# Kernel optimization log

Hardware: AMD Instinct MI355X
Metric: run time of the kernel (lower is better)

The kernel has to match this reference:

```python
import jax, jax.numpy as jnp
import numpy as np

E = 1024   # embd_size
H = 16     # heads_num
DH = E // H
DFF = 4 * E
B, T = 2, 2048


def layer_norm(x, g, b, eps=1e-5):
    mu = jnp.mean(x, axis=-1, keepdims=True)
    var = jnp.var(x, axis=-1, keepdims=True)
    return (x - mu) * jax.lax.rsqrt(var + eps) * g + b


def setup_inputs() -> dict:
    key = jax.random.key(0)
    ks = jax.random.split(key, 12)
    s = 0.02
    return {
        "x": jax.random.normal(ks[0], (B, T, E), dtype=jnp.float32),
        "Wq": jax.random.normal(ks[1], (E, E), dtype=jnp.float32) * s,
        "Wk": jax.random.normal(ks[2], (E, E), dtype=jnp.float32) * s,
        "Wv": jax.random.normal(ks[3], (E, E), dtype=jnp.float32) * s,
        "Wo": jax.random.normal(ks[4], (E, E), dtype=jnp.float32) * s,
        "bo": jnp.zeros((E,), dtype=jnp.float32),
        "W1": jax.random.normal(ks[5], (E, DFF), dtype=jnp.float32) * s,
        "b1": jnp.zeros((DFF,), dtype=jnp.float32),
        "W2": jax.random.normal(ks[6], (DFF, E), dtype=jnp.float32) * s,
        "b2": jnp.zeros((E,), dtype=jnp.float32),
        "g1": jnp.ones((E,), dtype=jnp.float32),
        "be1": jnp.zeros((E,), dtype=jnp.float32),
        "g2": jnp.ones((E,), dtype=jnp.float32),
        "be2": jnp.zeros((E,), dtype=jnp.float32),
    }


def reference(x, Wq, Wk, Wv, Wo, bo, W1, b1, W2, b2, g1, be1, g2, be2):
    Bx, Tx, C = x.shape
    # --- self-attention sublayer ---
    h = layer_norm(x, g1, be1)
    # per-head projections; heads concatenated along output dim == stacked weights
    q = (h @ Wq).reshape(Bx, Tx, H, DH)  # [B,T,H,Dh]
    k = (h @ Wk).reshape(Bx, Tx, H, DH)
    v = (h @ Wv).reshape(Bx, Tx, H, DH)
    # NOTE: original scales by full embd_size**-0.5 (C = x.shape[-1]), not head_size
    scale = C ** (-0.5)
    scores = jnp.einsum("bqhd,bkhd->bhqk", q, k) * scale  # [B,H,T,T]
    mask = jnp.tril(jnp.ones((Tx, Tx), dtype=bool))
    scores = jnp.where(mask, scores, -jnp.inf)
    attn = jax.nn.softmax(scores, axis=-1)
    o = jnp.einsum("bhqk,bkhd->bqhd", attn, v).reshape(Bx, Tx, C)
    sa = o @ Wo + bo
    x = x + sa
    # --- feed-forward sublayer ---
    h2 = layer_norm(x, g2, be2)
    ff = jax.nn.relu(h2 @ W1 + b1) @ W2 + b2
    return x + ff
```

## Files before the change

### kernel.cpp

```cpp
#include <hip/hip_runtime.h>
#include <hip/hip_bf16.h>
#include <math.h>

#define Bn 2
#define Tn 2048
#define En 1024
#define Hn 16
#define DFFn 4096
#define Mn (Bn*Tn)
#define QKVLD 3072

typedef __hip_bfloat16 bf16;
typedef unsigned short u16;
typedef unsigned int u32;
typedef __attribute__((ext_vector_type(8))) short short8;
typedef __attribute__((ext_vector_type(4))) float f32x4;

typedef __attribute__((address_space(1))) const void cg_void;
typedef __attribute__((address_space(3))) void lds_void;

#define QSC 0.0450842200278f

#define HBAR() asm volatile("s_waitcnt lgkmcnt(0)\n\ts_barrier" ::: "memory")

__device__ __forceinline__ u16 f2bf(float f) {
    bf16 h = __float2bfloat16(f);
    u16 u; __builtin_memcpy(&u, &h, 2); return u;
}
__device__ __forceinline__ float bf2f(u16 u) {
    u32 x = ((u32)u) << 16; float f; __builtin_memcpy(&f, &x, 4); return f;
}

__global__ __launch_bounds__(256)
void transpose_w4(const float* __restrict__ s0, const float* __restrict__ s1,
                  const float* __restrict__ s2, const float* __restrict__ s3,
                  u16* __restrict__ d0, u16* __restrict__ d1,
                  u16* __restrict__ d2, u16* __restrict__ d3) {
    const float* src = (blockIdx.z == 0) ? s0 : (blockIdx.z == 1) ? s1
                     : (blockIdx.z == 2) ? s2 : s3;
    u16* dst = (blockIdx.z == 0) ? d0 : (blockIdx.z == 1) ? d1
             : (blockIdx.z == 2) ? d2 : d3;
    __shared__ float t[64][65];
    const int r0 = blockIdx.y * 64, c0 = blockIdx.x * 64;
    const int tr = threadIdx.x >> 6, tc = threadIdx.x & 63;
#pragma unroll
    for (int i = 0; i < 16; i++)
        t[tr + i * 4][tc] = src[(size_t)(r0 + tr + i * 4) * 1024 + c0 + tc];
    __syncthreads();
#pragma unroll
    for (int i = 0; i < 16; i++)
        dst[(size_t)(c0 + tr + i * 4) * 1024 + r0 + tc] = f2bf(t[tc][tr + i * 4]);
}

__global__ __launch_bounds__(256)
void transpose_w(const float* __restrict__ src, u16* __restrict__ dst,
                 int R, int C) {
    __shared__ float t[64][65];
    const int r0 = blockIdx.y * 64, c0 = blockIdx.x * 64;
    const int tr = threadIdx.x >> 6, tc = threadIdx.x & 63;
#pragma unroll
    for (int i = 0; i < 16; i++)
        t[tr + i * 4][tc] = src[(size_t)(r0 + tr + i * 4) * C + c0 + tc];
    __syncthreads();
#pragma unroll
    for (int i = 0; i < 16; i++)
        dst[(size_t)(c0 + tr + i * 4) * R + r0 + tc] = f2bf(t[tc][tr + i * 4]);
}

__global__ __launch_bounds__(256)
void vcopy_t(const u16* __restrict__ QKV, u16* __restrict__ Vg) {
    const int bh = blockIdx.z;
    const int t0 = blockIdx.y * 64;
    __shared__ u16 t[64][65];
    const int tr = threadIdx.x >> 6, tc = threadIdx.x & 63;
    const u16* src = QKV + (size_t)(bh >> 4) * 2048 * QKVLD + 2048 + (bh & 15) * 64;
#pragma unroll
    for (int i = 0; i < 16; i++)
        t[tr + i * 4][tc] = src[(size_t)(t0 + tr + i * 4) * QKVLD + tc];
    __syncthreads();
    u16* dst = Vg + (size_t)bh * 64 * 2048;
#pragma unroll
    for (int i = 0; i < 16; i++)
        dst[(size_t)(tr + i * 4) * 2048 + t0 + tc] = t[tc][tr + i * 4];
}

template<typename AT>
__global__ __launch_bounds__(256)
void ln_kernel(const AT* __restrict__ x, const float* __restrict__ g,
               const float* __restrict__ b, u16* __restrict__ out) {
    const int row = blockIdx.x;
    const int tid = threadIdx.x;
    const AT* xp = x + (size_t)row * En;
    float v[4];
    float s = 0.f, sq = 0.f;
#pragma unroll
    for (int i = 0; i < 4; i++) {
        if constexpr (sizeof(AT) == 2) v[i] = bf2f(xp[tid + i * 256]);
        else                           v[i] = (float)xp[tid + i * 256];
        s += v[i];
        sq += v[i] * v[i];
    }
    __shared__ float rs[256], rq[256];
    rs[tid] = s; rq[tid] = sq;
    __syncthreads();
    for (int st = 128; st > 0; st >>= 1) {
        if (tid < st) { rs[tid] += rs[tid + st]; rq[tid] += rq[tid + st]; }
        __syncthreads();
    }
    const float mu  = rs[0] * (1.0f / En);
    const float var = rq[0] * (1.0f / En) - mu * mu;
    const float inv = rsqrtf(var + 1e-5f);
#pragma unroll
    for (int i = 0; i < 4; i++) {
        const int c = tid + i * 256;
        out[(size_t)row * En + c] = f2bf((v[i] - mu) * inv * g[c] + b[c]);
    }
}

__global__ __launch_bounds__(256)
void ff2_init(const u16* __restrict__ X1, const float* __restrict__ b2,
              float* __restrict__ out) {
    const int row = blockIdx.x;
    const int c = threadIdx.x * 4;
    ushort4 a = *(const ushort4*)&X1[(size_t)row * En + c];
    float4 bb = *(const float4*)&b2[c];
    float4 o;
    o.x = bf2f(a.x) + bb.x;
    o.y = bf2f(a.y) + bb.y;
    o.z = bf2f(a.z) + bb.z;
    o.w = bf2f(a.w) + bb.w;
    *(float4*)&out[(size_t)row * En + c] = o;
}

template<int TM, int HAS_BIAS, int RELU, int RES, int OUT_F32, int SCQ,
         int SPLITC, int SPLITA, int ATOM = 0, int XSWZ = 0, int PIPE = 0>
__global__ __launch_bounds__(256)
void gemm_bt(const u16* __restrict__ A, const u16* __restrict__ A2, int ldA,
             const u16* __restrict__ Wt, int ldW,
             const float* __restrict__ bias, const void* __restrict__ res,
             void* __restrict__ Cout, void* __restrict__ Cout2,
             int ldC, int Kd) {
    constexpr int IF = TM / 32;
    constexpr int LD = TM / 64 + 2;
    constexpr int RB = PIPE ? 4 : 1;
    __shared__ __align__(16) u16 As[RB][TM * 32];
    __shared__ __align__(16) u16 Bs[RB][128 * 32];
    const int tid  = threadIdx.x;
    const int lane = tid & 63, wv = tid >> 6;
    const int quad = lane >> 4, l16 = lane & 15;

    int bx = blockIdx.x, by = blockIdx.y, bz = blockIdx.z;
    if (XSWZ) {
        const int GX = gridDim.x, GY = gridDim.y;
        const int L = (bz * GY + by) * GX + bx;
        const int xcd = L & 7, slot = L >> 3;
        const int p = slot / GX;
        bx = slot - p * GX;
        const int yz = p * 8 + xcd;
        by = yz & (GY - 1);
        bz = yz >> __builtin_ctz(GY);
    }

    const int m0 = by * TM, n0 = bx * 128;
    const int rw = (wv >> 1) * (TM / 2), cw = (wv & 1) * 64;
    const int lr  = lane >> 2;
    const int gsw = ((lane & 3) ^ ((lane >> 3) & 3)) * 8;
    const int psw = (quad ^ ((l16 >> 1) & 3)) * 8;

    f32x4 acc[IF][4] = {};

    auto stage = [&](int buf, int kt) {
        const u16* Ap = (SPLITA && kt >= 2048) ? A2 : A;
        const int  kk = SPLITA ? (kt & 2047) : kt;
#pragma unroll
        for (int t = 0; t < TM / 64; t++) {
            const int row = wv * (TM / 4) + t * 16;
            __builtin_amdgcn_global_load_lds(
                (cg_void*)(const void*)&Ap[(size_t)(m0 + row + lr) * ldA + kk + gsw],
                (lds_void*)(void*)&As[buf][row * 32], 16, 0, 0);
        }
#pragma unroll
        for (int t = 0; t < 2; t++) {
            const int row = wv * 32 + t * 16;
            __builtin_amdgcn_global_load_lds(
                (cg_void*)(const void*)&Wt[(size_t)(n0 + row + lr) * ldW + kt + gsw],
                (lds_void*)(void*)&Bs[buf][row * 32], 16, 0, 0);
        }
    };
    auto compute = [&](int buf) {
        short8 af[IF], bfr[4];
#pragma unroll
        for (int i = 0; i < IF; i++)
            af[i] = *(const short8*)&As[buf][(rw + i * 16 + l16) * 32 + psw];
#pragma unroll
        for (int j = 0; j < 4; j++)
            bfr[j] = *(const short8*)&Bs[buf][(cw + j * 16 + l16) * 32 + psw];
#pragma unroll
        for (int i = 0; i < IF; i++)
#pragma unroll
            for (int j = 0; j < 4; j++)
                acc[i][j] = __builtin_amdgcn_mfma_f32_16x16x32_bf16(
                    af[i], bfr[j], acc[i][j], 0, 0, 0);
    };

    const int kbase = ATOM ? bz * Kd : 0;

    if constexpr (PIPE == 0) {
        for (int kt = kbase; kt < kbase + Kd; kt += 32) {
            __syncthreads();
            stage(0, kt);
            __syncthreads();
            compute(0);
        }
    } else {
        const int NI = Kd >> 5;
        stage(0, kbase);
        stage(1, kbase + 32);
        stage(2, kbase + 64);
        int bc = 0, bs = 3;
        for (int it = 0; it < NI; ++it) {
            if (it + 3 < NI) {
                stage(bs, kbase + (it + 3) * 32);
                if (++bs == RB) bs = 0;
            }
            const int rem = (NI - 1 - it) < 3 ? (NI - 1 - it) : 3;
            if (rem == 3) {
                if constexpr (LD == 4) asm volatile("s_waitcnt vmcnt(12)" ::: "memory");
                else                   asm volatile("s_waitcnt vmcnt(9)"  ::: "memory");
            } else if (rem == 2) {
                if constexpr (LD == 4) asm volatile("s_waitcnt vmcnt(8)"  ::: "memory");
                else                   asm volatile("s_waitcnt vmcnt(6)"  ::: "memory");
            } else if (rem == 1) {
                if constexpr (LD == 4) asm volatile("s_waitcnt vmcnt(4)"  ::: "memory");
                else                   asm volatile("s_waitcnt vmcnt(3)"  ::: "memory");
            } else {
                asm volatile("s_waitcnt vmcnt(0)" ::: "memory");
            }
            __builtin_amdgcn_s_barrier();
            compute(bc);
            if (++bc == RB) bc = 0;
            asm volatile("s_waitcnt lgkmcnt(0)" ::: "memory");
            __builtin_amdgcn_s_barrier();
        }
    }

    const float qscale = (SCQ && n0 < 1024) ? QSC : 1.0f;
    void* Cp = (SPLITC && n0 >= 2048) ? Cout2 : Cout;
#pragma unroll
    for (int i = 0; i < IF; i++) {
#pragma unroll
        for (int r = 0; r < 4; r++) {
            const int gm = m0 + rw + i * 16 + quad * 4 + r;
#pragma unroll
            for (int j = 0; j < 4; j++) {
                const int gn = n0 + cw + j * 16 + l16;
                const int cn = SPLITC ? (gn & 2047) : gn;
                float c = acc[i][j][r];
                if (HAS_BIAS) c += bias[gn];
                if (RELU) c = fmaxf(c, 0.f);
                if (RES == 1) c += ((const float*)res)[(size_t)gm * ldC + cn];
                if (RES == 2) c += bf2f(((const u16*)res)[(size_t)gm * ldC + cn]);
                if (SCQ) c *= qscale;
                if (ATOM) {
                    atomicAdd(&((float*)Cp)[(size_t)gm * ldC + cn], c);
                } else if (OUT_F32) {
                    ((float*)Cp)[(size_t)gm * ldC + cn] = c;
                } else {
                    ((u16*)Cp)[(size_t)gm * ldC + cn] = f2bf(c);
                }
            }
        }
    }
}

__global__ __launch_bounds__(256)
void flash_pass1(const u16* __restrict__ QKV, const u16* __restrict__ Vg,
                 u16* __restrict__ Op0, u16* __restrict__ Op1qkv,
                 float* __restrict__ stats) {
    const int pr = blockIdx.x >> 1, half = blockIdx.x & 1;
    const int hh = blockIdx.y, bb = blockIdx.z;
    const int tid  = threadIdx.x;
    const int lane = tid & 63, wv = tid >> 6;
    const int quad = lane >> 4, l16 = lane & 15;

    __shared__ __align__(16) u16 Ks[2][64 * 64];
    __shared__ __align__(16) u16 Vt[2][64 * 64];
    __shared__ __align__(16) u16 Ps[4][16 * 64];

    const size_t rowbase = (size_t)(bb * Tn) * QKVLD;
    const u16* Vgh = Vg + (size_t)(bb * Hn + hh) * 64 * 2048;

    const int sr = tid >> 2;
    const int p0 = (tid & 3) | ((sr & 1) << 2);
    const int p1 = p0 ^ 4;
    const int g0 = p0 ^ (sr & 7), g1 = p1 ^ (sr & 7);
    const int lsw = l16 & 7;

    uint4 kA, kB, vA, vB;
    auto prefetch = [&](int kt) {
        const size_t kb = rowbase + (size_t)(kt * 64 + sr) * QKVLD + 1024 + hh * 64;
        kA = *(const uint4*)&QKV[kb + g0 * 8];
        kB = *(const uint4*)&QKV[kb + g1 * 8];
        const size_t vb = (size_t)sr * 2048 + kt * 64;
        vA = *(const uint4*)&Vgh[vb + g0 * 8];
        vB = *(const uint4*)&Vgh[vb + g1 * 8];
    };
    auto writebuf = [&](int buf) {
        *(uint4*)&Ks[buf][sr * 64 + p0 * 8] = kA;
        *(uint4*)&Ks[buf][sr * 64 + p1 * 8] = kB;
        *(uint4*)&Vt[buf][sr * 64 + p0 * 8] = vA;
        *(uint4*)&Vt[buf][sr * 64 + p1 * 8] = vB;
    };

    for (int qsel = 0; qsel < 2; qsel++) {
        const int qt = qsel ? (31 - pr) : pr;
        const int nk = (qt >= half) ? ((qt - half) >> 1) + 1 : 0;
        const int qrow = qt * 64 + wv * 16 + l16;
        const int grow = bb * Tn + qrow;

        f32x4 ot[4] = {};
        float m2 = -INFINITY, lrow = 0.f;

        HBAR();
        if (nk > 0) {
            const u16* qp = QKV + rowbase + (size_t)qrow * QKVLD + hh * 64;
            short8 qf[2];
            qf[0] = *(const short8*)&qp[quad * 8];
            qf[1] = *(const short8*)&qp[32 + quad * 8];

            prefetch(half);
            writebuf(0);
            if (nk > 1) prefetch(half + 2);
            HBAR();

            const bool hasdiag = ((qt ^ half) & 1) == 0;
            for (int f = 0; f < nk; f++) {
                const int cur = f & 1;

                f32x4 st[4] = {};
#pragma unroll
                for (int ks = 0; ks < 2; ks++)
#pragma unroll
                    for (int i = 0; i < 4; i++) {
                        short8 kf = *(const short8*)&Ks[cur][(i * 16 + l16) * 64 +
                                     (((ks * 4 + quad) ^ lsw) * 8)];
                        st[i] = __builtin_amdgcn_mfma_f32_16x16x32_bf16(
                            kf, qf[ks], st[i], 0, 0, 0);
                    }

                float tmax = -INFINITY;
                if (hasdiag && f == nk - 1) {
                    const int qloc = wv * 16 + l16;
#pragma unroll
                    for (int i = 0; i < 4; i++)
#pragma unroll
                        for (int r = 0; r < 4; r++) {
                            float s = st[i][r];
                            if (i * 16 + quad * 4 + r > qloc) s = -INFINITY;
                            st[i][r] = s;
                            tmax = fmaxf(tmax, s);
                        }
                } else {
#pragma unroll
                    for (int i = 0; i < 4; i++)
#pragma unroll
                        for (int r = 0; r < 4; r++)
                            tmax = fmaxf(tmax, st[i][r]);
                }
                tmax = fmaxf(tmax, __shfl_xor(tmax, 16));
                tmax = fmaxf(tmax, __shfl_xor(tmax, 32));

                const float mnew = fmaxf(m2, tmax);
                const float alpha = exp2f(m2 - mnew);
                m2 = mnew;
                float psum = 0.f;
#pragma unroll
                for (int i = 0; i < 4; i++)
#pragma unroll
                    for (int r = 0; r < 4; r++) {
                        const float e = exp2f(st[i][r] - mnew);
                        st[i][r] = e;
                        psum += e;
                    }
                psum += __shfl_xor(psum, 16);
                psum += __shfl_xor(psum, 32);
                lrow = lrow * alpha + psum;
#pragma unroll
                for (int i = 0; i < 4; i++) ot[i] *= alpha;

#pragma unroll
                for (int i = 0; i < 4; i++) {
                    uint2 w;
                    w.x = (u32)f2bf(st[i][0]) | ((u32)f2bf(st[i][1]) << 16);
                    w.y = (u32)f2bf(st[i][2]) | ((u32)f2bf(st[i][3]) << 16);
                    const int g = (i * 2 + (quad >> 1)) ^ lsw;
                    *(uint2*)&Ps[wv][l16 * 64 + g * 8 + (quad & 1) * 4] = w;
                }
                asm volatile("s_waitcnt lgkmcnt(0)" ::: "memory");

#pragma unroll
                for (int ks = 0; ks < 2; ks++) {
                    short8 pf = *(const short8*)&Ps[wv][l16 * 64 +
                                 (((ks * 4 + quad) ^ lsw) * 8)];
#pragma unroll
                    for (int i = 0; i < 4; i++) {
                        short8 vf = *(const short8*)&Vt[cur][(i * 16 + l16) * 64 +
                                     (((ks * 4 + quad) ^ lsw) * 8)];
                        ot[i] = __builtin_amdgcn_mfma_f32_16x16x32_bf16(
                            vf, pf, ot[i], 0, 0, 0);
                    }
                }

                if (f + 1 < nk) {
                    writebuf(cur ^ 1);
                    if (f + 2 < nk) prefetch(half + 2 * (f + 2));
                    HBAR();
                }
            }
        }

        u16* op = (half == 0) ? (Op0 + (size_t)grow * 1024 + hh * 64)
                              : (Op1qkv + (size_t)grow * QKVLD + 2048 + hh * 64);
#pragma unroll
        for (int i = 0; i < 4; i++) {
            ushort4 o4;
            o4.x = f2bf(ot[i][0]); o4.y = f2bf(ot[i][1]);
            o4.z = f2bf(ot[i][2]); o4.w = f2bf(ot[i][3]);
            *(ushort4*)&op[i * 16 + quad * 4] = o4;
        }
        if (quad == 0) {
            stats[((size_t)(half * 2 + 0) * 4096 + grow) * 16 + hh] = m2;
            stats[((size_t)(half * 2 + 1) * 4096 + grow) * 16 + hh] = lrow;
        }
    }
}

__global__ __launch_bounds__(256)
void flash_merge(u16* __restrict__ QKV, const u16* __restrict__ Op0,
                 const float* __restrict__ stats) {
    const int row = blockIdx.x;
    const int tid = threadIdx.x;
    const int col = tid * 4;
    const int hh = col >> 6;
    const float m0 = stats[((size_t)0 * 4096 + row) * 16 + hh];
    const float l0 = stats[((size_t)1 * 4096 + row) * 16 + hh];
    const float m1 = stats[((size_t)2 * 4096 + row) * 16 + hh];
    const float l1 = stats[((size_t)3 * 4096 + row) * 16 + hh];
    const float m  = fmaxf(m0, m1);
    const float w0 = exp2f(m0 - m), w1 = exp2f(m1 - m);
    const float inv = 1.0f / (w0 * l0 + w1 * l1);
    ushort4 a = *(const ushort4*)&Op0[(size_t)row * 1024 + col];
    ushort4 b = *(const ushort4*)&QKV[(size_t)row * QKVLD + 2048 + col];
    ushort4 o;
    o.x = f2bf((w0 * bf2f(a.x) + w1 * bf2f(b.x)) * inv);
    o.y = f2bf((w0 * bf2f(a.y) + w1 * bf2f(b.y)) * inv);
    o.z = f2bf((w0 * bf2f(a.z) + w1 * bf2f(b.z)) * inv);
    o.w = f2bf((w0 * bf2f(a.w) + w1 * bf2f(b.w)) * inv);
    *(ushort4*)&QKV[(size_t)row * QKVLD + col] = o;
}

extern "C" void kernel_launch(void* const* d_in, const int* in_sizes, int n_in,
                              void* d_out, int out_size, void* d_ws, size_t ws_size,
                              hipStream_t stream) {
    const float* x   = (const float*)d_in[0];
    const float* Wq  = (const float*)d_in[1];
    const float* Wk  = (const float*)d_in[2];
    const float* Wv  = (const float*)d_in[3];
    const float* Wo  = (const float*)d_in[4];
    const float* bo  = (const float*)d_in[5];
    const float* W1  = (const float*)d_in[6];
    const float* b1  = (const float*)d_in[7];
    const float* W2  = (const float*)d_in[8];
    const float* b2  = (const float*)d_in[9];
    const float* g1  = (const float*)d_in[10];
    const float* be1 = (const float*)d_in[11];
    const float* g2  = (const float*)d_in[12];
    const float* be2 = (const float*)d_in[13];

    char* wsb = (char*)d_ws;
    u16*   QKV = (u16*)wsb;
    u16*   F1a = (u16*)wsb;
    u16*   W2T = (u16*)(wsb + 16u * 1024 * 1024);
    u16*   Op0 = (u16*)(wsb + 24u * 1024 * 1024);
    u16*   X1b = Op0;
    u16*   Vg  = (u16*)(wsb + 32u * 1024 * 1024);
    u16*   F1b = Vg;
    u16*   h     = (u16*)d_out;
    u16*   WT    = (u16*)((char*)d_out + 8u * 1024 * 1024);
    u16*   WqkvT = WT;
    u16*   WoT   = WT + 3u * 1024 * 1024;
    float* stats = (float*)WT;
    u16*   W1T   = WT;

    transpose_w4<<<dim3(16, 16, 4), 256, 0, stream>>>(
        Wq, Wk, Wv, Wo,
        WqkvT, WqkvT + 1024u * 1024, WqkvT + 2048u * 1024, WoT);

    ln_kernel<float><<<Mn, 256, 0, stream>>>(x, g1, be1, h);

    gemm_bt<128, 0, 0, 0, 0, 1, 0, 0, 0, 1, 0><<<dim3(24, 32), 256, 0, stream>>>(
        h, nullptr, En, WqkvT, En, nullptr, nullptr, QKV, nullptr, QKVLD, En);

    vcopy_t<<<dim3(1, 32, 32), 256, 0, stream>>>(QKV, Vg);

    flash_pass1<<<dim3(32, Hn, Bn), 256, 0, stream>>>(QKV, Vg, Op0, QKV, stats);

    flash_merge<<<Mn, 256, 0, stream>>>(QKV, Op0, stats);

    gemm_bt<64, 1, 0, 1, 0, 0, 0, 0, 0, 1, 0><<<dim3(8, 64), 256, 0, stream>>>(
        QKV, nullptr, QKVLD, WoT, En, bo, x, X1b, nullptr, En, En);

    transpose_w<<<dim3(64, 16), 256, 0, stream>>>(W1, W1T, 1024, 4096);
    transpose_w<<<dim3(16, 64), 256, 0, stream>>>(W2, W2T, 4096, 1024);

    ln_kernel<u16><<<Mn, 256, 0, stream>>>(X1b, g2, be2, h);

    gemm_bt<128, 1, 1, 0, 0, 0, 1, 0, 0, 1, 0><<<dim3(32, 32), 256, 0, stream>>>(
        h, nullptr, En, W1T, En, b1, nullptr, F1a, F1b, 2048, En);

    ff2_init<<<Mn, 256, 0, stream>>>(X1b, b2, (float*)d_out);

    gemm_bt<128, 0, 0, 0, 1, 0, 0, 1, 1, 1, 1><<<dim3(8, 32, 2), 256, 0, stream>>>(
        F1a, F1b, 2048, W2T, DFFn, nullptr, nullptr, (float*)d_out, nullptr,
        En, 2048);
}
```

Baseline: 388.0 us.

## Add 256x256-tile double-buffered GEMM kernel for FF1 projection

Adds a new gemm256 kernel with 512 threads, 256x256 output tiles, a K-step of 64, double-buffered LDS staging via global_load_lds with an XOR swizzle, and bf16 MFMA 16x16x32. It replaces the 128-tile gemm_bt launch for the W1 feed-forward GEMM. The larger tiles raise arithmetic intensity per LDS and global load. The trade-offs are 128 KB of LDS per block, high register pressure from a 32-fragment accumulator, and only 256 blocks to cover the device. The epilogue writes scalar, non-vectorized bf16 stores.

```diff
diff --git a/kernel.cpp b/kernel.cpp
--- a/kernel.cpp
+++ b/kernel.cpp
@@ -130,6 +130,95 @@
     o.z = bf2f(a.z) + bb.z;
     o.w = bf2f(a.w) + bb.w;
     *(float4*)&out[(size_t)row * En + c] = o;
+}
+
+template<int HAS_BIAS, int RELU, int SPLITC>
+__global__ __launch_bounds__(512, 2)
+void gemm256(const u16* __restrict__ A, int ldA,
+             const u16* __restrict__ Wt, int ldW,
+             const float* __restrict__ bias,
+             u16* __restrict__ Cout, u16* __restrict__ Cout2,
+             int ldC, int Kd) {
+    __shared__ __align__(16) u16 As[2][256 * 64];
+    __shared__ __align__(16) u16 Bs[2][256 * 64];
+    const int tid  = threadIdx.x;
+    const int lane = tid & 63, wv = tid >> 6;
+    const int quad = lane >> 4, l16 = lane & 15;
+    const int wr = wv >> 2, wc = wv & 3;
+    const int lr8 = lane >> 3;
+    const int gcg = (lane & 7) ^ lr8;
+
+    const int m0 = blockIdx.y * 256, n0 = blockIdx.x * 256;
+
+    f32x4 acc[8][4] = {};
+
+    auto stage = [&](int buf, int kt) {
+#pragma unroll
+        for (int i = 0; i < 4; i++) {
+            const int rbase = wv * 32 + i * 8;
+            __builtin_amdgcn_global_load_lds(
+                (cg_void*)(const void*)&A[(size_t)(m0 + rbase + lr8) * ldA + kt + gcg * 8],
+                (lds_void*)(void*)&As[buf][rbase * 64], 16, 0, 0);
+        }
+#pragma unroll
+        for (int i = 0; i < 4; i++) {
+            const int rbase = wv * 32 + i * 8;
+            __builtin_amdgcn_global_load_lds(
+                (cg_void*)(const void*)&Wt[(size_t)(n0 + rbase + lr8) * ldW + kt + gcg * 8],
+                (lds_void*)(void*)&Bs[buf][rbase * 64], 16, 0, 0);
+        }
+    };
+    auto compute = [&](int buf) {
+        const int swz = l16 & 7;
+#pragma unroll
+        for (int ks = 0; ks < 2; ks++) {
+            short8 a[8], b[4];
+#pragma unroll
+            for (int mf = 0; mf < 8; mf++)
+                a[mf] = *(const short8*)&As[buf][(wr * 128 + mf * 16 + l16) * 64 +
+                         (((ks * 4 + quad) ^ swz) * 8)];
+#pragma unroll
+            for (int nf = 0; nf < 4; nf++)
+                b[nf] = *(const short8*)&Bs[buf][(wc * 64 + nf * 16 + l16) * 64 +
+                         (((ks * 4 + quad) ^ swz) * 8)];
+#pragma unroll
+            for (int mf = 0; mf < 8; mf++)
+#pragma unroll
+                for (int nf = 0; nf < 4; nf++)
+                    acc[mf][nf] = __builtin_amdgcn_mfma_f32_16x16x32_bf16(
+                        a[mf], b[nf], acc[mf][nf], 0, 0, 0);
+        }
+    };
+
+    stage(0, 0);
+    asm volatile("s_waitcnt vmcnt(0)" ::: "memory");
+    __builtin_amdgcn_s_barrier();
+    const int NT = Kd >> 6;
+    for (int t = 0; t < NT; ++t) {
+        const int cur = t & 1;
+        if (t + 1 < NT) stage(cur ^ 1, (t + 1) * 64);
+        compute(cur);
+        asm volatile("s_waitcnt vmcnt(0) lgkmcnt(0)" ::: "memory");
+        __builtin_amdgcn_s_barrier();
+    }
+
+#pragma unroll
+    for (int mf = 0; mf < 8; mf++) {
+#pragma unroll
+        for (int r = 0; r < 4; r++) {
+            const int gm = m0 + wr * 128 + mf * 16 + quad * 4 + r;
+#pragma unroll
+            for (int nf = 0; nf < 4; nf++) {
+                const int gn = n0 + wc * 64 + nf * 16 + l16;
+                const int cn = SPLITC ? (gn & 2047) : gn;
+                float c = acc[mf][nf][r];
+                if (HAS_BIAS) c += bias[gn];
+                if (RELU) c = fmaxf(c, 0.f);
+                u16* Cp = (SPLITC && gn >= 2048) ? Cout2 : Cout;
+                Cp[(size_t)gm * ldC + cn] = f2bf(c);
+            }
+        }
+    }
 }
 
 template<int TM, int HAS_BIAS, int RELU, int RES, int OUT_F32, int SCQ,
@@ -515,8 +604,8 @@
 
     ln_kernel<u16><<<Mn, 256, 0, stream>>>(X1b, g2, be2, h);
 
-    gemm_bt<128, 1, 1, 0, 0, 0, 1, 0, 0, 1, 0><<<dim3(32, 32), 256, 0, stream>>>(
-        h, nullptr, En, W1T, En, b1, nullptr, F1a, F1b, 2048, En);
+    gemm256<1, 1, 1><<<dim3(16, 16), 512, 0, stream>>>(
+        h, En, W1T, En, b1, F1a, F1b, 2048, En);
 
     ff2_init<<<Mn, 256, 0, stream>>>(X1b, b2, (float*)d_out);
 
```

After: 373.1 us. 1.04x faster.
